# Kernel optimization log

Measured on AMD Instinct MI355X. Metric: run time of the kernel, lower is better.

Reference implementation:

```python
import jax, jax.numpy as jnp
import numpy as np

N_EMBD = 512
N_HEAD = 8
D_HEAD = N_EMBD // N_HEAD
N_EXPERTS = 4
TOP_K = 2
D_FF = 4 * N_EMBD
EPS_RMS = 1e-5


def setup_inputs() -> dict:
    key = jax.random.key(0)
    ks = jax.random.split(key, 10)
    B, T, C = 8, 1024, N_EMBD
    s = 0.02
    return {
        "x": jax.random.normal(ks[0], (B, T, C), jnp.float32),
        "ln1_w": jnp.ones((C,), jnp.float32),
        "ln2_w": jnp.ones((C,), jnp.float32),
        "wq": jax.random.normal(ks[1], (C, C), jnp.float32) * s,
        "wk": jax.random.normal(ks[2], (C, C), jnp.float32) * s,
        "wv": jax.random.normal(ks[3], (C, C), jnp.float32) * s,
        "wo": jax.random.normal(ks[4], (C, C), jnp.float32) * s,
        "gate_w": jax.random.normal(ks[5], (N_EXPERTS, C), jnp.float32) * s,
        "w_fc": jax.random.normal(ks[6], (N_EXPERTS, D_FF, C), jnp.float32) * s,
        "w_proj": jax.random.normal(ks[7], (N_EXPERTS, C, D_FF), jnp.float32) * s,
    }


def rms_norm(x, w):
    var = jnp.mean(x * x, axis=-1, keepdims=True)
    return x * jax.lax.rsqrt(var + EPS_RMS) * w


def causal_attention(x, wq, wk, wv, wo):
    B, T, C = x.shape
    q = (x @ wq.T).reshape(B, T, N_HEAD, D_HEAD)
    k = (x @ wk.T).reshape(B, T, N_HEAD, D_HEAD)
    v = (x @ wv.T).reshape(B, T, N_HEAD, D_HEAD)
    scores = jnp.einsum("bqhd,bkhd->bhqk", q, k) / jnp.sqrt(jnp.float32(D_HEAD))
    mask = jnp.tril(jnp.ones((T, T), bool))
    scores = jnp.where(mask, scores, jnp.finfo(scores.dtype).min)
    attn = jax.nn.softmax(scores, axis=-1)
    out = jnp.einsum("bhqk,bkhd->bqhd", attn, v).reshape(B, T, C)
    return out @ wo.T


def ds_moe(x, gate_w, w_fc, w_proj):
    B, T, C = x.shape
    xf = x.reshape(B * T, C)                                # [N, C]
    gate_logits = xf @ gate_w.T                             # [N, E]
    gate_probs = jax.nn.softmax(gate_logits, axis=-1)
    topw, topi = jax.lax.top_k(gate_probs, TOP_K)           # [N, K]
    topw = topw / jnp.clip(topw.sum(-1, keepdims=True), 1e-6)
    # sparse router weights [N, E] (scatter of normalized top-k)
    sparse_w = jnp.zeros((xf.shape[0], N_EXPERTS), xf.dtype)
    sparse_w = sparse_w.at[jnp.arange(xf.shape[0])[:, None], topi].set(topw)
    # dense-equivalent expert compute: out = sum_e w_e * MLP_e(x)
    h = jax.nn.gelu(jnp.einsum("nc,efc->enf", xf, w_fc), approximate=False)
    eo = jnp.einsum("enf,ecf->enc", h, w_proj)              # [E, N, C]
    out = jnp.einsum("ne,enc->nc", sparse_w, eo)
    return out.reshape(B, T, C), sparse_w


def reference(x, ln1_w, ln2_w, wq, wk, wv, wo, gate_w, w_fc, w_proj):
    x = x + causal_attention(rms_norm(x, ln1_w), wq, wk, wv, wo)
    moe_out, router_w = ds_moe(rms_norm(x, ln2_w), gate_w, w_fc, w_proj)
    x = x + moe_out
    return x, router_w
```

## Files before the change

### kernel.cpp

```cpp
#include <hip/hip_runtime.h>
#include <math.h>

typedef __bf16 bf16_t;
typedef float    f32x2 __attribute__((ext_vector_type(2)));
typedef float    f32x4 __attribute__((ext_vector_type(4)));
typedef unsigned u32x2 __attribute__((ext_vector_type(2)));
typedef unsigned u32x4 __attribute__((ext_vector_type(4)));
typedef __bf16   bf16x8 __attribute__((ext_vector_type(8)));

#define WS_MB (size_t)(1u << 20)

__device__ __forceinline__ void gl16(const bf16_t* g, bf16_t* l) {
    void* gnc = const_cast<void*>((const void*)g);
    __builtin_amdgcn_global_load_lds((__attribute__((address_space(1))) void*)gnc,
                                     (__attribute__((address_space(3))) void*)l,
                                     16, 0, 0);
}

__device__ __forceinline__ float dot4(f32x4 a, f32x4 b) {
    return a.x * b.x + a.y * b.y + a.z * b.z + a.w * b.w;
}

__device__ __forceinline__ int xcd_swz(int orig, int nwg) {
    int q = nwg >> 3, r = nwg & 7;
    int x = orig & 7, i = orig >> 3;
    int base = (x < r) ? x * (q + 1) : r * (q + 1) + (x - r) * q;
    return base + i;
}

__global__ __launch_bounds__(256) void cvt_all_kernel(
    const float* __restrict__ s0, const float* __restrict__ s1,
    const float* __restrict__ s2, const float* __restrict__ s3,
    const float* __restrict__ s4, const float* __restrict__ s5,
    bf16_t* __restrict__ d0, bf16_t* __restrict__ d1,
    bf16_t* __restrict__ d2, bf16_t* __restrict__ d3,
    bf16_t* __restrict__ d4, bf16_t* __restrict__ d5,
    int* __restrict__ cnt) {
    if (blockIdx.x == 0 && threadIdx.x < 4) cnt[threadIdx.x] = 0;
    int i = blockIdx.x * 256 + threadIdx.x;
    const float* s; bf16_t* d; int off;
    if (i < 262144) {
        int seg = i >> 16; off = i & 65535;
        s = seg == 0 ? s0 : seg == 1 ? s1 : seg == 2 ? s2 : s3;
        d = seg == 0 ? d0 : seg == 1 ? d1 : seg == 2 ? d2 : d3;
    } else if (i < 1310720) { s = s4; d = d4; off = i - 262144; }
    else                    { s = s5; d = d5; off = i - 1310720; }
    f32x4 v = ((const f32x4*)s)[off];
    union { bf16_t b[4]; u32x2 u; } p;
    p.b[0] = (bf16_t)v.x; p.b[1] = (bf16_t)v.y;
    p.b[2] = (bf16_t)v.z; p.b[3] = (bf16_t)v.w;
    ((u32x2*)d)[off] = p.u;
}

__global__ __launch_bounds__(256) void rmsnorm_kernel(const float* __restrict__ x,
                                                      const float* __restrict__ w,
                                                      bf16_t* __restrict__ out) {
    int row = blockIdx.x;
    const float* xr = x + (size_t)row * 512;
    int t = threadIdx.x;
    f32x2 v = *(const f32x2*)(xr + t * 2);
    float ss = v.x * v.x + v.y * v.y;
#pragma unroll
    for (int o = 32; o > 0; o >>= 1) ss += __shfl_down(ss, o);
    __shared__ float red[4];
    if ((t & 63) == 0) red[t >> 6] = ss;
    __syncthreads();
    float tot = (red[0] + red[1]) + (red[2] + red[3]);
    float sc = rsqrtf(tot * (1.0f / 512.0f) + 1e-5f);
    f32x2 wv = *(const f32x2*)(w + t * 2);
    union { bf16_t b[2]; unsigned u; } p;
    p.b[0] = (bf16_t)(v.x * sc * wv.x);
    p.b[1] = (bf16_t)(v.y * sc * wv.y);
    *(unsigned*)(out + (size_t)row * 512 + t * 2) = p.u;
}

__device__ inline float gelu_fast(float x) {
    float u = -1.5957691216f * x * fmaf(0.044715f * x, x, 1.0f);
    return x / (1.0f + __expf(u));
}

#define GEMM_COMPUTE(LA, LB)                                                          \
    _Pragma("unroll")                                                                 \
    for (int kk = 0; kk < 2; ++kk) {                                                  \
        bf16x8 af[4], bfr[4];                                                         \
        _Pragma("unroll")                                                             \
        for (int mi = 0; mi < 4; mi++)                                                \
            af[mi] = *(const bf16x8*)((LA) + (wr + mi * 16 + lrow) * 64               \
                                      + (((kk * 4 + sg) ^ lr3) * 8));                 \
        _Pragma("unroll")                                                             \
        for (int ni = 0; ni < 4; ni++)                                                \
            bfr[ni] = *(const bf16x8*)((LB) + (wc + ni * 16 + lrow) * 64              \
                                       + (((kk * 4 + sg) ^ lr3) * 8));                \
        _Pragma("unroll")                                                             \
        for (int mi = 0; mi < 4; mi++) {                                              \
            _Pragma("unroll")                                                         \
            for (int ni = 0; ni < 4; ni++) {                                          \
                acc[mi][ni] = __builtin_amdgcn_mfma_f32_16x16x32_bf16(                \
                    af[mi], bfr[ni], acc[mi][ni], 0, 0, 0);                           \
            }                                                                         \
        }                                                                             \
    }

template <int EPI>
__global__ __launch_bounds__(256) void gemm_kernel(const bf16_t* __restrict__ A,
                                                   const bf16_t* __restrict__ B,
                                                   void* __restrict__ C,
                                                   const float* __restrict__ aux,
                                                   int N, int K, int ncol) {
    const int id = xcd_swz(blockIdx.x, gridDim.x);
    const int row0 = (id / ncol) * 128;
    const int col0 = (id % ncol) * 128;
    __shared__ __align__(16) bf16_t lds_a[128 * 64];
    __shared__ __align__(16) bf16_t lds_b[128 * 64];
    const int t = threadIdx.x;
    const bf16_t* Ap = A + (size_t)row0 * K;
    const bf16_t* Bp = B + (size_t)col0 * K;
    const int lane = t & 63, wave = t >> 6;
    const int wr = (wave >> 1) * 64, wc = (wave & 1) * 64;
    const int lrow = lane & 15;
    const int sg = lane >> 4, lr3 = lane & 7;
    const int srow = lane >> 3;
    const int scolx = ((lane & 7) ^ (lane >> 3)) * 8;

    f32x4 acc[4][4];
    f32x4 zero = {0.f, 0.f, 0.f, 0.f};
#pragma unroll
    for (int i = 0; i < 4; i++)
#pragma unroll
        for (int j = 0; j < 4; j++) acc[i][j] = zero;

    for (int k0 = 0; k0 < K; k0 += 64) {
        __syncthreads();
#pragma unroll
        for (int c = 0; c < 4; ++c) {
            const int rbase = wave * 32 + c * 8;
            gl16(Ap + (size_t)(rbase + srow) * K + k0 + scolx, lds_a + rbase * 64);
            gl16(Bp + (size_t)(rbase + srow) * K + k0 + scolx, lds_b + rbase * 64);
        }
        __syncthreads();
        GEMM_COMPUTE(lds_a, lds_b)
    }

#pragma unroll
    for (int mi = 0; mi < 4; mi++) {
        int rbase = row0 + wr + mi * 16 + (lane >> 4) * 4;
#pragma unroll
        for (int ni = 0; ni < 4; ni++) {
            int col = col0 + wc + ni * 16 + (lane & 15);
#pragma unroll
            for (int r = 0; r < 4; r++) {
                float v = acc[mi][ni][r];
                size_t idx = (size_t)(rbase + r) * N + col;
                if (EPI == 1) ((float*)C)[idx] = v + aux[idx];
                else          ((bf16_t*)C)[idx] = (bf16_t)v;
            }
        }
    }
}

__global__ __launch_bounds__(256) void moe_fc_kernel(
    const bf16_t* __restrict__ A, const bf16_t* __restrict__ B, bf16_t* __restrict__ H,
    const int* __restrict__ list, const int* __restrict__ cnt, const int* __restrict__ seg) {
    const int id = xcd_swz(blockIdx.x, gridDim.x);
    const int row0g = (id >> 4) * 128;
    const int col0 = (id & 15) * 128;
    int e = 0;
    if (row0g >= seg[1]) e = 1;
    if (row0g >= seg[2]) e = 2;
    if (row0g >= seg[3]) e = 3;
    const int ce = cnt[e];
    const int rl0 = row0g - seg[e];
    if (rl0 >= ce) return;

    __shared__ __align__(16) bf16_t lds_a[128 * 64];
    __shared__ __align__(16) bf16_t lds_b[128 * 64];
    const int t = threadIdx.x;
    const bf16_t* Bp = B + ((size_t)e * 2048 + col0) * 512;
    const int* le = list + e * 8192;
    const int lane = t & 63, wave = t >> 6;
    const int wr = (wave >> 1) * 64, wc = (wave & 1) * 64;
    const int lrow = lane & 15;
    const int sg = lane >> 4, lr3 = lane & 7;
    const int srow = lane >> 3;
    const int scolx = ((lane & 7) ^ (lane >> 3)) * 8;

    const bf16_t* Asrc[4];
#pragma unroll
    for (int c = 0; c < 4; ++c) {
        int r = rl0 + wave * 32 + c * 8 + srow;
        r = (r < ce) ? r : (ce - 1);
        Asrc[c] = A + (size_t)le[r] * 512 + scolx;
    }

    f32x4 acc[4][4];
    f32x4 zero = {0.f, 0.f, 0.f, 0.f};
#pragma unroll
    for (int i = 0; i < 4; i++)
#pragma unroll
        for (int j = 0; j < 4; j++) acc[i][j] = zero;

    for (int k0 = 0; k0 < 512; k0 += 64) {
        __syncthreads();
#pragma unroll
        for (int c = 0; c < 4; ++c) {
            const int rbase = wave * 32 + c * 8;
            gl16(Asrc[c] + k0, lds_a + rbase * 64);
            gl16(Bp + (size_t)(rbase + srow) * 512 + k0 + scolx, lds_b + rbase * 64);
        }
        __syncthreads();
        GEMM_COMPUTE(lds_a, lds_b)
    }

#pragma unroll
    for (int mi = 0; mi < 4; mi++) {
        int rbase = row0g + wr + mi * 16 + (lane >> 4) * 4;
#pragma unroll
        for (int ni = 0; ni < 4; ni++) {
            int col = col0 + wc + ni * 16 + (lane & 15);
#pragma unroll
            for (int r = 0; r < 4; r++) {
                H[(size_t)(rbase + r) * 2048 + col] = (bf16_t)gelu_fast(acc[mi][ni][r]);
            }
        }
    }
}

__global__ __launch_bounds__(256) void moe_pj_kernel(
    const bf16_t* __restrict__ H, const bf16_t* __restrict__ B, float* __restrict__ xout,
    const float* __restrict__ rw, const int* __restrict__ list,
    const int* __restrict__ cnt, const int* __restrict__ seg) {
    const int id = xcd_swz(blockIdx.x, gridDim.x);
    const int row0g = (id >> 3) * 128;
    const int col0 = (id & 7) * 64;
    int e = 0;
    if (row0g >= seg[1]) e = 1;
    if (row0g >= seg[2]) e = 2;
    if (row0g >= seg[3]) e = 3;
    const int ce = cnt[e];
    const int se = seg[e];
    const int rl0 = row0g - se;
    if (rl0 >= ce) return;

    __shared__ __align__(16) bf16_t lds_a[128 * 64];
    __shared__ __align__(16) bf16_t lds_b[64 * 64];
    const int t = threadIdx.x;
    const bf16_t* Ap = H + (size_t)row0g * 2048;
    const bf16_t* Bp = B + ((size_t)e * 512 + col0) * 2048;
    const int* le = list + e * 8192;
    const int lane = t & 63, wave = t >> 6;
    const int wr = (wave >> 1) * 64, wc = (wave & 1) * 32;
    const int lrow = lane & 15;
    const int sg = lane >> 4, lr3 = lane & 7;
    const int srow = lane >> 3;
    const int scolx = ((lane & 7) ^ (lane >> 3)) * 8;

    f32x4 acc[4][2];
    f32x4 zero = {0.f, 0.f, 0.f, 0.f};
#pragma unroll
    for (int i = 0; i < 4; i++)
#pragma unroll
        for (int j = 0; j < 2; j++) acc[i][j] = zero;

    for (int k0 = 0; k0 < 2048; k0 += 64) {
        __syncthreads();
#pragma unroll
        for (int c = 0; c < 4; ++c) {
            const int rbase = wave * 32 + c * 8;
            gl16(Ap + (size_t)(rbase + srow) * 2048 + k0 + scolx, lds_a + rbase * 64);
        }
        {
            const int rbase = wave * 16;
            gl16(Bp + (size_t)(rbase + srow) * 2048 + k0 + scolx, lds_b + rbase * 64);
            gl16(Bp + (size_t)(rbase + 8 + srow) * 2048 + k0 + scolx, lds_b + (rbase + 8) * 64);
        }
        __syncthreads();
#pragma unroll
        for (int kk = 0; kk < 2; ++kk) {
            bf16x8 af[4], bfr[2];
#pragma unroll
            for (int mi = 0; mi < 4; mi++)
                af[mi] = *(const bf16x8*)(lds_a + (wr + mi * 16 + lrow) * 64
                                          + (((kk * 4 + sg) ^ lr3) * 8));
#pragma unroll
            for (int ni = 0; ni < 2; ni++)
                bfr[ni] = *(const bf16x8*)(lds_b + (wc + ni * 16 + lrow) * 64
                                           + (((kk * 4 + sg) ^ lr3) * 8));
#pragma unroll
            for (int mi = 0; mi < 4; mi++) {
#pragma unroll
                for (int ni = 0; ni < 2; ni++) {
                    acc[mi][ni] = __builtin_amdgcn_mfma_f32_16x16x32_bf16(
                        af[mi], bfr[ni], acc[mi][ni], 0, 0, 0);
                }
            }
        }
    }

#pragma unroll
    for (int mi = 0; mi < 4; mi++) {
        int rbase = row0g + wr + mi * 16 + (lane >> 4) * 4;
#pragma unroll
        for (int ni = 0; ni < 2; ni++) {
            int col = col0 + wc + ni * 16 + (lane & 15);
#pragma unroll
            for (int r = 0; r < 4; r++) {
                int rloc = rbase + r - se;
                if (rloc < ce) {
                    int tok = le[rloc];
                    atomicAdd(xout + (size_t)tok * 512 + col,
                              rw[(size_t)tok * 4 + e] * acc[mi][ni][r]);
                }
            }
        }
    }
}

__global__ __launch_bounds__(256) void attn_kernel(const bf16_t* __restrict__ QKV,
                                                   bf16_t* __restrict__ O) {
    __shared__ __align__(16) bf16_t klds[2 * 64 * 32];
    __shared__ __align__(16) bf16_t vlds[4 * 2 * 16 * 32];

    const int bx = blockIdx.x;
    const int qb = 15 - (bx >> 6);
    const int bh = bx & 63;
    const int b = bh >> 3, h = bh & 7;
    const int t = threadIdx.x;
    const int lane = t & 63, wave = t >> 6;
    const int g = lane >> 4, q15 = lane & 15;
    const int qbase = qb * 64 + wave * 16;
    const int qabs = qbase + q15;

    const bf16_t* Qb = QKV + (size_t)b * 1024 * 1536 + h * 64;
    const bf16_t* Kb = Qb + 512;
    const bf16_t* Vb = Qb + 1024;

    const bf16_t* qp = Qb + (size_t)qabs * 1536 + g * 8;
    bf16x8 qf0 = *(const bf16x8*)(qp);
    bf16x8 qf1 = *(const bf16x8*)(qp + 32);

    f32x4 acc[4];
    f32x4 zero = {0.f, 0.f, 0.f, 0.f};
#pragma unroll
    for (int i = 0; i < 4; i++) acc[i] = zero;
    float m = -1e30f, denom = 0.f;

    const int kr1 = t >> 3, kc1 = t & 7;
    const int vr = t & 63, vc1 = t >> 6, vc2 = vc1 + 4;
    const int perm = ((q15 >> 2) * 8) + (q15 & 3);

    const int nkt = qb + 1;
    for (int kt = 0; kt < nkt; ++kt) {
        u32x4 ka  = *(const u32x4*)(Kb + (size_t)(kt * 64 + kr1) * 1536 + kc1 * 8);
        u32x4 kb2 = *(const u32x4*)(Kb + (size_t)(kt * 64 + kr1 + 32) * 1536 + kc1 * 8);
        u32x4 va  = *(const u32x4*)(Vb + (size_t)(kt * 64 + vr) * 1536 + vc1 * 8);
        u32x4 vb2 = *(const u32x4*)(Vb + (size_t)(kt * 64 + vr) * 1536 + vc2 * 8);
        __syncthreads();
        *(u32x4*)(klds + (kc1 >> 2) * 2048 + kr1 * 32 + (kc1 & 3) * 8) = ka;
        *(u32x4*)(klds + (kc1 >> 2) * 2048 + (kr1 + 32) * 32 + (kc1 & 3) * 8) = kb2;
        {
            union { u32x4 u; bf16_t e[8]; } tv;
            const int kh = vr >> 5, k32 = vr & 31;
            tv.u = va;
#pragma unroll
            for (int j = 0; j < 8; ++j) {
                int d = vc1 * 8 + j;
                vlds[(((d >> 4) * 2 + kh) * 16 + (d & 15)) * 32 + k32] = tv.e[j];
            }
            tv.u = vb2;
#pragma unroll
            for (int j = 0; j < 8; ++j) {
                int d = vc2 * 8 + j;
                vlds[(((d >> 4) * 2 + kh) * 16 + (d & 15)) * 32 + k32] = tv.e[j];
            }
        }
        __syncthreads();

        for (int s32 = 0; s32 < 2; ++s32) {
            const int KB = kt * 64 + s32 * 32;
            if (KB > qbase + 15) break;
            const int r0 = s32 * 32 + perm;
            bf16x8 k00 = *(const bf16x8*)(klds + r0 * 32 + g * 8);
            bf16x8 k01 = *(const bf16x8*)(klds + 2048 + r0 * 32 + g * 8);
            bf16x8 k10 = *(const bf16x8*)(klds + (r0 + 4) * 32 + g * 8);
            bf16x8 k11 = *(const bf16x8*)(klds + 2048 + (r0 + 4) * 32 + g * 8);
            f32x4 s0 = zero, s1 = zero;
            s0 = __builtin_amdgcn_mfma_f32_16x16x32_bf16(k00, qf0, s0, 0, 0, 0);
            s0 = __builtin_amdgcn_mfma_f32_16x16x32_bf16(k01, qf1, s0, 0, 0, 0);
            s1 = __builtin_amdgcn_mfma_f32_16x16x32_bf16(k10, qf0, s1, 0, 0, 0);
            s1 = __builtin_amdgcn_mfma_f32_16x16x32_bf16(k11, qf1, s1, 0, 0, 0);

            const int kbg = KB + 8 * g;
            float sv[8];
#pragma unroll
            for (int r = 0; r < 4; ++r) {
                sv[r]     = (kbg + r     <= qabs) ? s0[r] * 0.125f : -1e30f;
                sv[4 + r] = (kbg + 4 + r <= qabs) ? s1[r] * 0.125f : -1e30f;
            }
            float tm = sv[0];
#pragma unroll
            for (int j = 1; j < 8; ++j) tm = fmaxf(tm, sv[j]);
            tm = fmaxf(tm, __shfl_xor(tm, 16));
            tm = fmaxf(tm, __shfl_xor(tm, 32));
            const float mn = fmaxf(m, tm);
            const float co = __expf(m - mn);
            float p[8];
            float ts = 0.f;
#pragma unroll
            for (int j = 0; j < 8; ++j) { p[j] = __expf(sv[j] - mn); ts += p[j]; }
            ts += __shfl_xor(ts, 16);
            ts += __shfl_xor(ts, 32);
            denom = denom * co + ts;
            m = mn;
            union { bf16_t e[8]; bf16x8 v; } pp;
#pragma unroll
            for (int j = 0; j < 8; ++j) pp.e[j] = (bf16_t)p[j];

#pragma unroll
            for (int db = 0; db < 4; ++db) {
                acc[db] *= co;
                bf16x8 vf = *(const bf16x8*)(vlds + ((db * 2 + s32) * 16 + q15) * 32 + g * 8);
                acc[db] = __builtin_amdgcn_mfma_f32_16x16x32_bf16(vf, pp.v, acc[db], 0, 0, 0);
            }
        }
    }

    const float inv = 1.0f / denom;
    bf16_t* op = O + (size_t)b * 1024 * 512 + h * 64 + (size_t)qabs * 512;
#pragma unroll
    for (int db = 0; db < 4; ++db) {
        union { bf16_t e[4]; u32x2 u; } w;
#pragma unroll
        for (int r = 0; r < 4; ++r) w.e[r] = (bf16_t)(acc[db][r] * inv);
        *(u32x2*)(op + db * 16 + g * 4) = w.u;
    }
}

__global__ void seg_kernel(const int* __restrict__ cnt, int* __restrict__ seg) {
    if (threadIdx.x == 0) {
        int b = 0;
#pragma unroll
        for (int e = 0; e < 4; ++e) { seg[e] = b; b += (cnt[e] + 127) & ~127; }
    }
}

__global__ __launch_bounds__(256) void router_kernel(
    const float* __restrict__ xr, const float* __restrict__ w,
    const float* __restrict__ gw, bf16_t* __restrict__ hb,
    float* __restrict__ rout, int* __restrict__ list, int* __restrict__ cnt) {
    __shared__ int lcnt[4], gb[4];
    __shared__ int ent_tok[64], ent_e[64], ent_r[64];
    const int t = threadIdx.x, lane = t & 63, wave = t >> 6;
    if (t < 4) lcnt[t] = 0;
    __syncthreads();

    const f32x4 w0  = *(const f32x4*)(w + lane * 8);
    const f32x4 w1  = *(const f32x4*)(w + lane * 8 + 4);
    const f32x4 g00 = *(const f32x4*)(gw + lane * 8);
    const f32x4 g01 = *(const f32x4*)(gw + lane * 8 + 4);
    const f32x4 g10 = *(const f32x4*)(gw + 512 + lane * 8);
    const f32x4 g11 = *(const f32x4*)(gw + 512 + lane * 8 + 4);
    const f32x4 g20 = *(const f32x4*)(gw + 1024 + lane * 8);
    const f32x4 g21 = *(const f32x4*)(gw + 1024 + lane * 8 + 4);
    const f32x4 g30 = *(const f32x4*)(gw + 1536 + lane * 8);
    const f32x4 g31 = *(const f32x4*)(gw + 1536 + lane * 8 + 4);

    for (int it = 0; it < 8; ++it) {
        const int tok = blockIdx.x * 32 + wave * 8 + it;
        const float* row = xr + (size_t)tok * 512 + lane * 8;
        f32x4 v0 = *(const f32x4*)(row);
        f32x4 v1 = *(const f32x4*)(row + 4);
        float ss = dot4(v0, v0) + dot4(v1, v1);
        f32x4 xw0, xw1;
        xw0.x = v0.x * w0.x; xw0.y = v0.y * w0.y; xw0.z = v0.z * w0.z; xw0.w = v0.w * w0.w;
        xw1.x = v1.x * w1.x; xw1.y = v1.y * w1.y; xw1.z = v1.z * w1.z; xw1.w = v1.w * w1.w;
        float d0 = dot4(xw0, g00) + dot4(xw1, g01);
        float d1 = dot4(xw0, g10) + dot4(xw1, g11);
        float d2 = dot4(xw0, g20) + dot4(xw1, g21);
        float d3 = dot4(xw0, g30) + dot4(xw1, g31);
#pragma unroll
        for (int o = 32; o > 0; o >>= 1) {
            ss += __shfl_xor(ss, o);
            d0 += __shfl_xor(d0, o);
            d1 += __shfl_xor(d1, o);
            d2 += __shfl_xor(d2, o);
            d3 += __shfl_xor(d3, o);
        }
        const float sc = rsqrtf(ss * (1.0f / 512.0f) + 1e-5f);
        union { bf16_t b[8]; u32x4 u; } hw;
        hw.b[0] = (bf16_t)(xw0.x * sc); hw.b[1] = (bf16_t)(xw0.y * sc);
        hw.b[2] = (bf16_t)(xw0.z * sc); hw.b[3] = (bf16_t)(xw0.w * sc);
        hw.b[4] = (bf16_t)(xw1.x * sc); hw.b[5] = (bf16_t)(xw1.y * sc);
        hw.b[6] = (bf16_t)(xw1.z * sc); hw.b[7] = (bf16_t)(xw1.w * sc);
        *(u32x4*)(hb + (size_t)tok * 512 + lane * 8) = hw.u;

        const float l0 = d0 * sc, l1 = d1 * sc, l2 = d2 * sc, l3 = d3 * sc;
        float mx = fmaxf(fmaxf(l0, l1), fmaxf(l2, l3));
        float p[4];
        p[0] = expf(l0 - mx); p[1] = expf(l1 - mx);
        p[2] = expf(l2 - mx); p[3] = expf(l3 - mx);
        float s = (p[0] + p[1]) + (p[2] + p[3]);
        float is = 1.0f / s;
        p[0] *= is; p[1] *= is; p[2] *= is; p[3] *= is;
        int i0 = 0; float b0 = p[0];
#pragma unroll
        for (int e = 1; e < 4; e++) if (p[e] > b0) { b0 = p[e]; i0 = e; }
        int i1 = -1; float b1 = -1.f;
#pragma unroll
        for (int e = 0; e < 4; e++) {
            if (e == i0) continue;
            if (p[e] > b1) { b1 = p[e]; i1 = e; }
        }
        if (lane == 0) {
            float inv2 = 1.0f / fmaxf(b0 + b1, 1e-6f);
            float o[4] = {0.f, 0.f, 0.f, 0.f};
            o[i0] = b0 * inv2;
            o[i1] = b1 * inv2;
            f32x4 ov; ov.x = o[0]; ov.y = o[1]; ov.z = o[2]; ov.w = o[3];
            *(f32x4*)(rout + (size_t)tok * 4) = ov;
            int r0 = atomicAdd(&lcnt[i0], 1);
            int r1 = atomicAdd(&lcnt[i1], 1);
            int ei = (wave * 8 + it) * 2;
            ent_tok[ei] = tok;     ent_e[ei] = i0;     ent_r[ei] = r0;
            ent_tok[ei + 1] = tok; ent_e[ei + 1] = i1; ent_r[ei + 1] = r1;
        }
    }
    __syncthreads();
    if (t < 4) gb[t] = atomicAdd(&cnt[t], lcnt[t]);
    __syncthreads();
    if (t < 64) {
        int e = ent_e[t];
        list[e * 8192 + gb[e] + ent_r[t]] = ent_tok[t];
    }
}

extern "C" void kernel_launch(void* const* d_in, const int* in_sizes, int n_in,
                              void* d_out, int out_size, void* d_ws, size_t ws_size,
                              hipStream_t stream) {
    (void)in_sizes; (void)n_in; (void)out_size; (void)ws_size;
    const float* x   = (const float*)d_in[0];
    const float* ln1 = (const float*)d_in[1];
    const float* ln2 = (const float*)d_in[2];
    const float* wq  = (const float*)d_in[3];
    const float* wk  = (const float*)d_in[4];
    const float* wv  = (const float*)d_in[5];
    const float* wo  = (const float*)d_in[6];
    const float* gw  = (const float*)d_in[7];
    const float* wfc = (const float*)d_in[8];
    const float* wpj = (const float*)d_in[9];

    char* ws = (char*)d_ws;
    bf16_t* hb    = (bf16_t*)(ws);
    bf16_t* qkvb  = (bf16_t*)(ws + 8 * WS_MB);
    bf16_t* attb  = (bf16_t*)(ws + 32 * WS_MB);
    bf16_t* Hb    = (bf16_t*)(ws + 8 * WS_MB);
    bf16_t* wqkvb = (bf16_t*)(ws + 74 * WS_MB);
    bf16_t* wob   = (bf16_t*)(ws + 74 * WS_MB + 1536 * 1024);
    bf16_t* wfcb  = (bf16_t*)(ws + 76 * WS_MB);
    bf16_t* wpjb  = (bf16_t*)(ws + 84 * WS_MB);
    int*    list  = (int*)(ws + 92 * WS_MB);
    int*    cnt   = (int*)(ws + 92 * WS_MB + 192 * 1024);
    int*    seg   = cnt + 8;

    float* xout   = (float*)d_out;
    float* router = xout + (size_t)8192 * 512;

    cvt_all_kernel<<<9216, 256, 0, stream>>>(wq, wk, wv, wo, wfc, wpj,
                                             wqkvb, wqkvb + 512 * 512, wqkvb + 1024 * 512,
                                             wob, wfcb, wpjb, cnt);

    rmsnorm_kernel<<<8192, 256, 0, stream>>>(x, ln1, hb);
    gemm_kernel<4><<<768, 256, 0, stream>>>(hb, wqkvb, (void*)qkvb, nullptr, 1536, 512, 12);

    attn_kernel<<<1024, 256, 0, stream>>>(qkvb, attb);

    gemm_kernel<1><<<256, 256, 0, stream>>>(attb, wob, (void*)xout, x, 512, 512, 4);

    router_kernel<<<256, 256, 0, stream>>>(xout, ln2, gw, hb, router, list, cnt);
    seg_kernel<<<1, 64, 0, stream>>>(cnt, seg);

    moe_fc_kernel<<<16 * 131, 256, 0, stream>>>(hb, wfcb, Hb, list, cnt, seg);
    moe_pj_kernel<<<8 * 131, 256, 0, stream>>>(Hb, wpjb, xout, router, list, cnt, seg);
}
```

Before: 266.3 us.

## Double-buffer LDS tiles in MoE projection GEMM to overlap loads with MFMA

Splits the LDS tiles of the MoE down-projection kernel into two buffers, so the next K-slice is fetched with global_load_lds while the current slice is computed. Each iteration now ends with one vmcnt wait and a barrier, replacing the two __syncthreads per step. The cost is twice the LDS per block (48KB), which may lower occupancy, and it relies on the manual s_waitcnt placement being correct.

```diff
diff --git a/kernel.cpp b/kernel.cpp
--- a/kernel.cpp
+++ b/kernel.cpp
@@ -225,6 +225,43 @@
     }
 }
 
+#define PJ_VMCNT0() asm volatile("s_waitcnt vmcnt(0)" ::: "memory")
+
+#define PJ_STAGE(LA, LB, kk0)                                                          \
+    _Pragma("unroll")                                                                  \
+    for (int c = 0; c < 4; ++c) {                                                      \
+        const int rbase = wave * 32 + c * 8;                                           \
+        gl16(Ap + (size_t)(rbase + srow) * 2048 + (kk0) + scolx, (LA) + rbase * 64);   \
+    }                                                                                  \
+    {                                                                                  \
+        const int rbase = wave * 16;                                                   \
+        gl16(Bp + (size_t)(rbase + srow) * 2048 + (kk0) + scolx, (LB) + rbase * 64);   \
+        gl16(Bp + (size_t)(rbase + 8 + srow) * 2048 + (kk0) + scolx,                   \
+             (LB) + (rbase + 8) * 64);                                                 \
+    }
+
+#define PJ_COMPUTE(LA, LB)                                                             \
+    _Pragma("unroll")                                                                  \
+    for (int kk = 0; kk < 2; ++kk) {                                                   \
+        bf16x8 af[4], bfr[2];                                                          \
+        _Pragma("unroll")                                                              \
+        for (int mi = 0; mi < 4; mi++)                                                 \
+            af[mi] = *(const bf16x8*)((LA) + (wr + mi * 16 + lrow) * 64                \
+                                      + (((kk * 4 + sg) ^ lr3) * 8));                  \
+        _Pragma("unroll")                                                              \
+        for (int ni = 0; ni < 2; ni++)                                                 \
+            bfr[ni] = *(const bf16x8*)((LB) + (wc + ni * 16 + lrow) * 64               \
+                                       + (((kk * 4 + sg) ^ lr3) * 8));                 \
+        _Pragma("unroll")                                                              \
+        for (int mi = 0; mi < 4; mi++) {                                               \
+            _Pragma("unroll")                                                          \
+            for (int ni = 0; ni < 2; ni++) {                                           \
+                acc[mi][ni] = __builtin_amdgcn_mfma_f32_16x16x32_bf16(                 \
+                    af[mi], bfr[ni], acc[mi][ni], 0, 0, 0);                            \
+            }                                                                          \
+        }                                                                              \
+    }
+
 __global__ __launch_bounds__(256) void moe_pj_kernel(
     const bf16_t* __restrict__ H, const bf16_t* __restrict__ B, float* __restrict__ xout,
     const float* __restrict__ rw, const int* __restrict__ list,
@@ -241,8 +278,10 @@
     const int rl0 = row0g - se;
     if (rl0 >= ce) return;
 
-    __shared__ __align__(16) bf16_t lds_a[128 * 64];
-    __shared__ __align__(16) bf16_t lds_b[64 * 64];
+    __shared__ __align__(16) bf16_t lds_a0[128 * 64];
+    __shared__ __align__(16) bf16_t lds_a1[128 * 64];
+    __shared__ __align__(16) bf16_t lds_b0[64 * 64];
+    __shared__ __align__(16) bf16_t lds_b1[64 * 64];
     const int t = threadIdx.x;
     const bf16_t* Ap = H + (size_t)row0g * 2048;
     const bf16_t* Bp = B + ((size_t)e * 512 + col0) * 2048;
@@ -261,39 +300,19 @@
 #pragma unroll
         for (int j = 0; j < 2; j++) acc[i][j] = zero;
 
-    for (int k0 = 0; k0 < 2048; k0 += 64) {
-        __syncthreads();
-#pragma unroll
-        for (int c = 0; c < 4; ++c) {
-            const int rbase = wave * 32 + c * 8;
-            gl16(Ap + (size_t)(rbase + srow) * 2048 + k0 + scolx, lds_a + rbase * 64);
-        }
-        {
-            const int rbase = wave * 16;
-            gl16(Bp + (size_t)(rbase + srow) * 2048 + k0 + scolx, lds_b + rbase * 64);
-            gl16(Bp + (size_t)(rbase + 8 + srow) * 2048 + k0 + scolx, lds_b + (rbase + 8) * 64);
-        }
-        __syncthreads();
-#pragma unroll
-        for (int kk = 0; kk < 2; ++kk) {
-            bf16x8 af[4], bfr[2];
-#pragma unroll
-            for (int mi = 0; mi < 4; mi++)
-                af[mi] = *(const bf16x8*)(lds_a + (wr + mi * 16 + lrow) * 64
-                                          + (((kk * 4 + sg) ^ lr3) * 8));
-#pragma unroll
-            for (int ni = 0; ni < 2; ni++)
-                bfr[ni] = *(const bf16x8*)(lds_b + (wc + ni * 16 + lrow) * 64
-                                           + (((kk * 4 + sg) ^ lr3) * 8));
-#pragma unroll
-            for (int mi = 0; mi < 4; mi++) {
-#pragma unroll
-                for (int ni = 0; ni < 2; ni++) {
-                    acc[mi][ni] = __builtin_amdgcn_mfma_f32_16x16x32_bf16(
-                        af[mi], bfr[ni], acc[mi][ni], 0, 0, 0);
-                }
-            }
-        }
+    PJ_STAGE(lds_a0, lds_b0, 0)
+    PJ_VMCNT0();
+    __builtin_amdgcn_s_barrier();
+
+    for (int k0 = 0; k0 < 2048; k0 += 128) {
+        PJ_STAGE(lds_a1, lds_b1, k0 + 64)
+        PJ_COMPUTE(lds_a0, lds_b0)
+        PJ_VMCNT0();
+        __builtin_amdgcn_s_barrier();
+        if (k0 + 128 < 2048) { PJ_STAGE(lds_a0, lds_b0, k0 + 128) }
+        PJ_COMPUTE(lds_a1, lds_b1)
+        PJ_VMCNT0();
+        __builtin_amdgcn_s_barrier();
     }
 
 #pragma unroll
```

Measured after the change: 265.6 us. About the same (-0.3%).
